# Optimization experiments

Hardware: AMD Instinct MI355X
Metric: run time of the kernel (lower is better)

## Reference

```python
import jax, jax.numpy as jnp
import numpy as np

K = 3
STRIDE = 2
SQRT_D = 4  # in_d_capsules = 16 -> 4x4 matrix pose
LN_EPS = 1e-5


def _unfold(x, k, s):
    # x: [B, N, H, W, A] -> [B, N, k, k, Hout, Wout, A] (matches torch unfold+permute)
    B, N, H, W, A = x.shape
    Hout = (H - k) // s + 1
    Wout = (W - k) // s + 1
    hi = jnp.arange(Hout) * s
    wi = jnp.arange(Wout) * s
    x1 = x[:, :, hi[:, None] + jnp.arange(k)[None, :]]            # [B,N,Hout,k,W,A]
    x2 = x1[:, :, :, :, wi[:, None] + jnp.arange(k)[None, :]]     # [B,N,Hout,k,Wout,k,A]
    return jnp.transpose(x2, (0, 1, 3, 5, 2, 4, 6))               # [B,N,k,k,Hout,Wout,A]


def setup_inputs() -> dict:
    key = jax.random.key(0)
    k1, k2, k3 = jax.random.split(key, 3)
    B, N_in, H, W, D_in = 32, 32, 32, 32, 16
    N_out, D_out = 32, 16
    Hout = (H - K) // STRIDE + 1
    Wout = (W - K) // STRIDE + 1
    w_const = np.sqrt(N_out / (SQRT_D * N_in * K * K)).astype(np.float32)
    return {
        "input": jax.random.normal(k1, (B, N_in, H, W, D_in), dtype=jnp.float32),
        "next_capsule_value": jax.random.normal(k2, (B, N_out, Hout, Wout, D_out), dtype=jnp.float32),
        "w": w_const * jax.random.normal(k3, (K, K, N_in, SQRT_D, SQRT_D, N_out), dtype=jnp.float32),
        "gamma": jnp.ones((D_out,), dtype=jnp.float32),
        "beta": jnp.zeros((D_out,), dtype=jnp.float32),
        "num_iter": 1,
    }


def reference(input, next_capsule_value, w, gamma, beta, num_iter):
    out_d = SQRT_D * SQRT_D
    scale = 1.0 / np.sqrt(out_d).astype(np.float32)
    inp = _unfold(input, K, STRIDE)                                # [B,N,k,k,h,w,A]
    B, N, _, _, h, wd, A = inp.shape
    _inp = inp.reshape(B, N, K, K, h, wd, SQRT_D, SQRT_D)          # bnklhwax
    M = next_capsule_value.shape[1]
    ncv = next_capsule_value.reshape(B, M, h, wd, SQRT_D, SQRT_D)  # bmhwad
    # query-key routing logits
    qk = jnp.einsum('bnklhwax,klnxdm,bmhwad->bnklmhw', _inp, w, ncv) * scale
    qk = jax.nn.softmax(qk, axis=4)
    qk = qk / (jnp.sum(qk, axis=4, keepdims=True) + 1e-10)
    # value aggregation
    out = jnp.einsum('bnklmhw,bnklhwax,klnxdm->bmhwad', qk, _inp, w)
    out = out.reshape(B, M, h, wd, out_d)
    # dropout p=0 -> identity; LayerNorm over capsule dim
    mu = jnp.mean(out, axis=-1, keepdims=True)
    var = jnp.var(out, axis=-1, keepdims=True)
    out = (out - mu) / jnp.sqrt(var + LN_EPS) * gamma + beta
    return out
```

## Files before the change

### kernel.cpp

```cpp
#include <hip/hip_runtime.h>

#define HOUT 15
#define WOUT 15

#define ASG __attribute__((address_space(1)))
#define ASL __attribute__((address_space(3)))

typedef float v2 __attribute__((ext_vector_type(2)));

__global__ __launch_bounds__(256, 2) void caps_part(
    const float* __restrict__ input,
    const float* __restrict__ ncv,
    const float* __restrict__ wt,
    float* __restrict__ part0,
    float* __restrict__ part1)
{
    __shared__ float lw[2][4608];

    const int tid   = threadIdx.x;
    const int grp   = tid >> 5;
    const int lane  = tid & 31;
    const int wv    = tid >> 6;
    const int wlane = tid & 63;

    const int pos = blockIdx.x * 8 + grp;
    const int b   = pos / (HOUT * WOUT);
    const int hw  = pos % (HOUT * WOUT);
    const int h   = hw / WOUT;
    const int wo  = hw % WOUT;

    const int s  = blockIdx.y;
    const int n0 = s * 16;

    auto stage = [&](int n, int buf) {
        for (int t = wv; t < 18; t += 4) {
            const int c = t >> 1, half = t & 1;
            const float* src = wt + c * 16384 + n * 512 + half * 256 + wlane * 4;
            float* dst = &lw[buf][c * 512 + half * 256];
            __builtin_amdgcn_global_load_lds((const ASG void*)src, (ASL void*)dst,
                                             16, 0, 0);
        }
    };

    stage(n0, 0);

    const float* ncv_p = ncv + ((((size_t)b * 32 + lane) * HOUT + h) * WOUT + wo) * 16;
    v2 cv2[8];
#pragma unroll
    for (int j = 0; j < 8; ++j) cv2[j] = *(const v2*)(ncv_p + j * 2);

    v2 acc2[8];
#pragma unroll
    for (int j = 0; j < 8; ++j) acc2[j] = (v2){0.0f, 0.0f};

    const int h0 = h * 2, w0 = wo * 2;

    __syncthreads();

    for (int i = 0; i < 16; ++i) {
        const int n = n0 + i;
        if (i + 1 < 16) stage(n + 1, (i + 1) & 1);

        const float* wbuf = lw[i & 1];
        const float* ipn  = input + ((((size_t)b * 32 + n) * 32 + h0) * 32 + w0) * 16;

#pragma unroll
        for (int k = 0; k < 3; ++k) {
#pragma unroll
            for (int l = 0; l < 3; ++l) {
                const int kl = k * 3 + l;
                const float* ip = ipn + (k * 32 + l) * 16;
                float av[16];
#pragma unroll
                for (int j = 0; j < 16; j += 4) {
                    float4 t = *(const float4*)(ip + j);
                    av[j] = t.x; av[j + 1] = t.y; av[j + 2] = t.z; av[j + 3] = t.w;
                }

                const float* wp = wbuf + kl * 512 + lane;

                v2 u2[8];
#pragma unroll
                for (int j = 0; j < 8; ++j) u2[j] = (v2){0.0f, 0.0f};
#pragma unroll
                for (int x = 0; x < 4; ++x) {
                    float wd0 = wp[(x * 4 + 0) * 32];
                    float wd1 = wp[(x * 4 + 1) * 32];
                    float wd2 = wp[(x * 4 + 2) * 32];
                    float wd3 = wp[(x * 4 + 3) * 32];
                    v2 wlo = {wd0, wd1};
                    v2 whi = {wd2, wd3};
#pragma unroll
                    for (int a = 0; a < 4; ++a) {
                        v2 sp = {av[a * 4 + x], av[a * 4 + x]};
                        u2[a * 2 + 0] = __builtin_elementwise_fma(sp, wlo, u2[a * 2 + 0]);
                        u2[a * 2 + 1] = __builtin_elementwise_fma(sp, whi, u2[a * 2 + 1]);
                    }
                }

                v2 d0 = {0.f, 0.f}, d1 = {0.f, 0.f};
#pragma unroll
                for (int j = 0; j < 4; ++j) {
                    d0 = __builtin_elementwise_fma(u2[j],     cv2[j],     d0);
                    d1 = __builtin_elementwise_fma(u2[j + 4], cv2[j + 4], d1);
                }
                v2 dd = d0 + d1;
                float logit = (dd.x + dd.y) * 0.25f;

                float e = __expf(logit);
                float sum = e;
#pragma unroll
                for (int o = 16; o > 0; o >>= 1)
                    sum += __shfl_xor(sum, o, 32);
                float p = e * __builtin_amdgcn_rcpf(sum);
                v2 p2 = {p, p};

#pragma unroll
                for (int j = 0; j < 8; ++j)
                    acc2[j] = __builtin_elementwise_fma(p2, u2[j], acc2[j]);
            }
        }

        if (i < 15) __syncthreads();
    }

    float* op = (s == 0 ? part0 : part1)
              + ((((size_t)b * 32 + lane) * HOUT + h) * WOUT + wo) * 16;
#pragma unroll
    for (int j = 0; j < 4; ++j) {
        float4 r;
        r.x = acc2[2 * j].x;     r.y = acc2[2 * j].y;
        r.z = acc2[2 * j + 1].x; r.w = acc2[2 * j + 1].y;
        *(float4*)(op + j * 4) = r;
    }
}

__global__ __launch_bounds__(256) void caps_ln(
    const float* __restrict__ part1,
    const float* __restrict__ gamma,
    const float* __restrict__ beta,
    float* __restrict__ out)
{
    const size_t t = (size_t)blockIdx.x * 256 + threadIdx.x;
    const float* p0 = out   + t * 16;
    const float* p1 = part1 + t * 16;

    float a[16];
#pragma unroll
    for (int j = 0; j < 16; j += 4) {
        float4 x = *(const float4*)(p0 + j);
        float4 y = *(const float4*)(p1 + j);
        a[j] = x.x + y.x; a[j+1] = x.y + y.y; a[j+2] = x.z + y.z; a[j+3] = x.w + y.w;
    }

    float mu = 0.0f;
#pragma unroll
    for (int j = 0; j < 16; ++j) mu += a[j];
    mu *= 0.0625f;
    float var = 0.0f;
#pragma unroll
    for (int j = 0; j < 16; ++j) { float d = a[j] - mu; var = fmaf(d, d, var); }
    var *= 0.0625f;
    float rstd = __builtin_amdgcn_rsqf(var + 1e-5f);

    float* op = out + t * 16;
#pragma unroll
    for (int j = 0; j < 16; j += 4) {
        float4 g  = *(const float4*)(gamma + j);
        float4 be = *(const float4*)(beta + j);
        float4 r;
        r.x = (a[j + 0] - mu) * rstd * g.x + be.x;
        r.y = (a[j + 1] - mu) * rstd * g.y + be.y;
        r.z = (a[j + 2] - mu) * rstd * g.z + be.z;
        r.w = (a[j + 3] - mu) * rstd * g.w + be.w;
        *(float4*)(op + j) = r;
    }
}

extern "C" void kernel_launch(void* const* d_in, const int* in_sizes, int n_in,
                              void* d_out, int out_size, void* d_ws, size_t ws_size,
                              hipStream_t stream) {
    const float* input = (const float*)d_in[0];
    const float* ncv   = (const float*)d_in[1];
    const float* wt    = (const float*)d_in[2];
    const float* gamma = (const float*)d_in[3];
    const float* beta  = (const float*)d_in[4];
    float* out  = (float*)d_out;
    float* ws   = (float*)d_ws;

    caps_part<<<dim3(900, 2), dim3(256), 0, stream>>>(input, ncv, wt, out, ws);
    caps_ln<<<dim3(900), dim3(256), 0, stream>>>(ws, gamma, beta, out);
}
```

Measured before the change: 377.5 us.

## Pre-transpose weights, read them from global memory, and reduce halves with atomics

A new small kernel transposes the weight tensor into a workspace. Each lane's 16 weight values for a (n, kl, m) triple become contiguous, so the main kernel reads them with four float4 global loads. This drops the double-buffered LDS staging and the per-iteration __syncthreads. The two channel halves no longer go to separate partial buffers: they are atomically added into a zeroed output, and the LayerNorm kernel reads only that buffer. The trade-off is a memset, an extra transpose launch and float atomics. Weight reads also now go through the vector cache instead of LDS, with every group in a block re-reading the same data.

```diff
diff --git a/kernel.cpp b/kernel.cpp
--- a/kernel.cpp
+++ b/kernel.cpp
@@ -3,25 +3,39 @@
 #define HOUT 15
 #define WOUT 15
 
-#define ASG __attribute__((address_space(1)))
-#define ASL __attribute__((address_space(3)))
+typedef float v2 __attribute__((ext_vector_type(2)));
 
-typedef float v2 __attribute__((ext_vector_type(2)));
+__global__ __launch_bounds__(256) void w_transpose(
+    const float* __restrict__ wt, float* __restrict__ wT)
+{
+    const int t = blockIdx.x * 256 + threadIdx.x;
+    const int n  = t / 288;
+    const int r  = t % 288;
+    const int kl = r >> 5;
+    const int m  = r & 31;
+
+    const float* src = wt + kl * 16384 + n * 512 + m;
+    float v[16];
+#pragma unroll
+    for (int xd = 0; xd < 16; ++xd) v[xd] = src[xd * 32];
+
+    float* dst = wT + (size_t)t * 16;
+#pragma unroll
+    for (int j = 0; j < 4; ++j) {
+        float4 o = {v[4 * j], v[4 * j + 1], v[4 * j + 2], v[4 * j + 3]};
+        *(float4*)(dst + 4 * j) = o;
+    }
+}
 
 __global__ __launch_bounds__(256, 2) void caps_part(
     const float* __restrict__ input,
     const float* __restrict__ ncv,
-    const float* __restrict__ wt,
-    float* __restrict__ part0,
-    float* __restrict__ part1)
+    const float* __restrict__ wT,
+    float* __restrict__ out)
 {
-    __shared__ float lw[2][4608];
-
-    const int tid   = threadIdx.x;
-    const int grp   = tid >> 5;
-    const int lane  = tid & 31;
-    const int wv    = tid >> 6;
-    const int wlane = tid & 63;
+    const int tid  = threadIdx.x;
+    const int grp  = tid >> 5;
+    const int lane = tid & 31;
 
     const int pos = blockIdx.x * 8 + grp;
     const int b   = pos / (HOUT * WOUT);
@@ -29,20 +43,7 @@
     const int h   = hw / WOUT;
     const int wo  = hw % WOUT;
 
-    const int s  = blockIdx.y;
-    const int n0 = s * 16;
-
-    auto stage = [&](int n, int buf) {
-        for (int t = wv; t < 18; t += 4) {
-            const int c = t >> 1, half = t & 1;
-            const float* src = wt + c * 16384 + n * 512 + half * 256 + wlane * 4;
-            float* dst = &lw[buf][c * 512 + half * 256];
-            __builtin_amdgcn_global_load_lds((const ASG void*)src, (ASL void*)dst,
-                                             16, 0, 0);
-        }
-    };
-
-    stage(n0, 0);
+    const int n0 = blockIdx.y * 16;
 
     const float* ncv_p = ncv + ((((size_t)b * 32 + lane) * HOUT + h) * WOUT + wo) * 16;
     v2 cv2[8];
@@ -55,14 +56,10 @@
 
     const int h0 = h * 2, w0 = wo * 2;
 
-    __syncthreads();
-
     for (int i = 0; i < 16; ++i) {
         const int n = n0 + i;
-        if (i + 1 < 16) stage(n + 1, (i + 1) & 1);
-
-        const float* wbuf = lw[i & 1];
-        const float* ipn  = input + ((((size_t)b * 32 + n) * 32 + h0) * 32 + w0) * 16;
+        const float* ipn = input + ((((size_t)b * 32 + n) * 32 + h0) * 32 + w0) * 16;
+        const float* wn  = wT + ((size_t)n * 288 + lane) * 16;
 
 #pragma unroll
         for (int k = 0; k < 3; ++k) {
@@ -77,19 +74,18 @@
                     av[j] = t.x; av[j + 1] = t.y; av[j + 2] = t.z; av[j + 3] = t.w;
                 }
 
-                const float* wp = wbuf + kl * 512 + lane;
+                const float* wr = wn + kl * 512;
+                float4 wv[4];
+#pragma unroll
+                for (int x = 0; x < 4; ++x) wv[x] = *(const float4*)(wr + 4 * x);
 
                 v2 u2[8];
 #pragma unroll
                 for (int j = 0; j < 8; ++j) u2[j] = (v2){0.0f, 0.0f};
 #pragma unroll
                 for (int x = 0; x < 4; ++x) {
-                    float wd0 = wp[(x * 4 + 0) * 32];
-                    float wd1 = wp[(x * 4 + 1) * 32];
-                    float wd2 = wp[(x * 4 + 2) * 32];
-                    float wd3 = wp[(x * 4 + 3) * 32];
-                    v2 wlo = {wd0, wd1};
-                    v2 whi = {wd2, wd3};
+                    v2 wlo = {wv[x].x, wv[x].y};
+                    v2 whi = {wv[x].z, wv[x].w};
 #pragma unroll
                     for (int a = 0; a < 4; ++a) {
                         v2 sp = {av[a * 4 + x], av[a * 4 + x]};
@@ -120,37 +116,29 @@
                     acc2[j] = __builtin_elementwise_fma(p2, u2[j], acc2[j]);
             }
         }
-
-        if (i < 15) __syncthreads();
     }
 
-    float* op = (s == 0 ? part0 : part1)
-              + ((((size_t)b * 32 + lane) * HOUT + h) * WOUT + wo) * 16;
+    float* op = out + ((((size_t)b * 32 + lane) * HOUT + h) * WOUT + wo) * 16;
 #pragma unroll
-    for (int j = 0; j < 4; ++j) {
-        float4 r;
-        r.x = acc2[2 * j].x;     r.y = acc2[2 * j].y;
-        r.z = acc2[2 * j + 1].x; r.w = acc2[2 * j + 1].y;
-        *(float4*)(op + j * 4) = r;
+    for (int j = 0; j < 8; ++j) {
+        atomicAdd(op + 2 * j,     acc2[j].x);
+        atomicAdd(op + 2 * j + 1, acc2[j].y);
     }
 }
 
 __global__ __launch_bounds__(256) void caps_ln(
-    const float* __restrict__ part1,
     const float* __restrict__ gamma,
     const float* __restrict__ beta,
     float* __restrict__ out)
 {
     const size_t t = (size_t)blockIdx.x * 256 + threadIdx.x;
-    const float* p0 = out   + t * 16;
-    const float* p1 = part1 + t * 16;
+    float* op = out + t * 16;
 
     float a[16];
 #pragma unroll
     for (int j = 0; j < 16; j += 4) {
-        float4 x = *(const float4*)(p0 + j);
-        float4 y = *(const float4*)(p1 + j);
-        a[j] = x.x + y.x; a[j+1] = x.y + y.y; a[j+2] = x.z + y.z; a[j+3] = x.w + y.w;
+        float4 x = *(const float4*)(op + j);
+        a[j] = x.x; a[j + 1] = x.y; a[j + 2] = x.z; a[j + 3] = x.w;
     }
 
     float mu = 0.0f;
@@ -163,7 +151,6 @@
     var *= 0.0625f;
     float rstd = __builtin_amdgcn_rsqf(var + 1e-5f);
 
-    float* op = out + t * 16;
 #pragma unroll
     for (int j = 0; j < 16; j += 4) {
         float4 g  = *(const float4*)(gamma + j);
@@ -185,9 +172,11 @@
     const float* wt    = (const float*)d_in[2];
     const float* gamma = (const float*)d_in[3];
     const float* beta  = (const float*)d_in[4];
-    float* out  = (float*)d_out;
-    float* ws   = (float*)d_ws;
+    float* out = (float*)d_out;
+    float* wT  = (float*)d_ws;
 
-    caps_part<<<dim3(900, 2), dim3(256), 0, stream>>>(input, ncv, wt, out, ws);
-    caps_ln<<<dim3(900), dim3(256), 0, stream>>>(ws, gamma, beta, out);
+    hipMemsetAsync(out, 0, (size_t)out_size * sizeof(float), stream);
+    w_transpose<<<dim3(36), dim3(256), 0, stream>>>(wt, wT);
+    caps_part<<<dim3(900, 2), dim3(256), 0, stream>>>(input, ncv, wT, out);
+    caps_ln<<<dim3(900), dim3(256), 0, stream>>>(gamma, beta, out);
 }
```

Measured after the change: 762.1 us. 102% more time.
